# Performance work log

Measured on AMD Instinct MI355X. Metric: run time of the kernel, lower is better.

## Reference

```python
import jax, jax.numpy as jnp
import numpy as np
from jax import lax

BATCH, FS, DIM = 32, 7, 512
E, TOPK, KD = 4, 2, 4            # experts, top-k, scan directions
N_STATE, DT_RANK = 16, 32
CAP_FACTOR, EPS, AUX_W = 1.25, 1e-6, 0.01


def _layernorm(x, g, b, eps=1e-5):
    mu = x.mean(-1, keepdims=True)
    var = ((x - mu) ** 2).mean(-1, keepdims=True)
    return (x - mu) * lax.rsqrt(var + eps) * g + b


def setup_inputs() -> dict:
    key = jax.random.key(0)
    ks = jax.random.split(key, 10)
    s = 0.02
    d = DIM
    return {
        "x": jax.random.normal(ks[0], (BATCH, FS, FS, d), jnp.float32),
        "w_gate": jax.random.normal(ks[1], (d, E)) * s,
        "b_gate": jnp.zeros((E,), jnp.float32),
        "in_proj_w": jax.random.normal(ks[2], (E, d, 2 * d)) * s,
        "in_proj_b": jnp.zeros((E, 2 * d), jnp.float32),
        "conv_w": jax.random.normal(ks[3], (E, d, 3, 3)) * s,
        "conv_b": jnp.zeros((E, d), jnp.float32),
        "x_proj_w": jax.random.normal(ks[4], (E, KD, DT_RANK + 2 * N_STATE, d)) * s,
        "dt_proj_w": jax.random.normal(ks[5], (E, KD, d, DT_RANK)) * s,
        "dt_proj_b": jax.random.normal(ks[6], (E, KD, d)) * 0.1,
        "A_log": jnp.log(jax.random.uniform(ks[7], (E, KD, d, N_STATE), minval=1.0, maxval=16.0)),
        "Ds": jnp.ones((E, KD, d), jnp.float32),
        "out_norm_g": jnp.ones((E, d), jnp.float32),
        "out_norm_b": jnp.zeros((E, d), jnp.float32),
        "norm_g": jnp.ones((E, d), jnp.float32),
        "norm_b": jnp.zeros((E, d), jnp.float32),
    }


def _ss2d_expert(x, in_w, in_b, cw, cb, xpw, dtw, dtb, A_log, Ds, og, ob, ng, nb):
    # x: [B,H,W,d]; one SS2D expert (VMamba-style, use_out_proj=False, out_norm=True)
    B, H, W, d = x.shape
    L = H * W
    xz = x @ in_w + in_b                      # [B,H,W,2d]
    xin, z = jnp.split(xz, 2, axis=-1)
    xc = jnp.transpose(xin, (0, 3, 1, 2))     # [B,d,H,W]
    xc = lax.conv_general_dilated(xc, cw[:, None, :, :], (1, 1), 'SAME',
                                  feature_group_count=d,
                                  dimension_numbers=('NCHW', 'OIHW', 'NCHW'))
    xc = jax.nn.silu(xc + cb[None, :, None, None])
    xh = xc.reshape(B, d, L)                              # row-major (h)
    xv = jnp.transpose(xc, (0, 1, 3, 2)).reshape(B, d, L)  # col-major (v)
    xs = jnp.stack([xh, xh[..., ::-1], xv, xv[..., ::-1]], axis=1)  # [B,K,d,L]

    x_dbl = jnp.einsum('bkdl,kcd->bkcl', xs, xpw)
    dt, Bm, Cm = jnp.split(x_dbl, [DT_RANK, DT_RANK + N_STATE], axis=2)
    dt = jnp.einsum('bkrl,kdr->bkdl', dt, dtw) + dtb[None, :, :, None]
    dt = jax.nn.softplus(dt)                  # [B,K,d,L]
    A = -jnp.exp(A_log)                       # [K,d,N]

    def step(h, inp):
        dt_t, B_t, C_t, x_t = inp             # [B,K,d],[B,K,N],[B,K,N],[B,K,d]
        h = h * jnp.exp(dt_t[..., None] * A) + (dt_t * x_t)[..., None] * B_t[:, :, None, :]
        y = jnp.einsum('bkdn,bkn->bkd', h, C_t)
        return h, y

    h0 = jnp.zeros((B, KD, d, N_STATE), x.dtype)
    seq = (jnp.moveaxis(dt, 3, 0), jnp.moveaxis(Bm, 3, 0),
           jnp.moveaxis(Cm, 3, 0), jnp.moveaxis(xs, 3, 0))
    _, ys = lax.scan(step, h0, seq)           # [L,B,K,d]
    ys = jnp.moveaxis(ys, 0, 3) + Ds[None, :, :, None] * xs  # [B,K,d,L]

    y = ys[:, 0] + ys[:, 1, :, ::-1]
    yv = ys[:, 2] + ys[:, 3, :, ::-1]
    y = y + jnp.transpose(yv.reshape(B, d, W, H), (0, 1, 3, 2)).reshape(B, d, L)
    y = jnp.transpose(y.reshape(B, d, H, W), (0, 2, 3, 1))   # [B,H,W,d]
    y = _layernorm(y, og, ob) * jax.nn.silu(z)
    pooled = y.mean(axis=(1, 2))              # adaptive avg pool -> [B,d]
    return _layernorm(pooled, ng, nb)


def reference(x, w_gate, b_gate, in_proj_w, in_proj_b, conv_w, conv_b, x_proj_w,
              dt_proj_w, dt_proj_b, A_log, Ds, out_norm_g, out_norm_b, norm_g, norm_b):
    B = x.shape[0]
    # gate on globally pooled features
    x_flat = x.mean(axis=(1, 2))                              # [B,dim]
    raw = jax.nn.softmax(x_flat @ w_gate + b_gate, axis=-1)   # [B,E]
    capacity = int(CAP_FACTOR * B)
    _, idx = lax.top_k(raw, TOPK)
    mask = jax.nn.one_hot(idx, E, dtype=raw.dtype).sum(axis=1)  # [B,E]
    masked = raw * mask
    denom = masked.sum(0, keepdims=True) + EPS
    gate_scores = masked / denom * capacity
    importance = raw.mean(0)
    load = mask.mean(0)
    aux_loss = AUX_W * jnp.mean((load - importance) ** 2)

    topv, topi = lax.top_k(gate_scores, TOPK)                 # [B,k]
    # dense dispatch: run every expert on the full batch (E small), then gather
    all_out = jax.vmap(_ss2d_expert, in_axes=(None,) + (0,) * 13)(
        x, in_proj_w, in_proj_b, conv_w, conv_b, x_proj_w, dt_proj_w, dt_proj_b,
        A_log, Ds, out_norm_g, out_norm_b, norm_g, norm_b)    # [E,B,dim]
    sel = all_out[topi, jnp.arange(B)[:, None]]               # [B,k,dim]
    mixed = (topv[..., None] * sel).sum(axis=1)               # [B,dim]
    return mixed, aux_loss
```

## Files before the change

### kernel.cpp

```cpp
#include <hip/hip_runtime.h>
#include <hip/hip_bf16.h>

#define B_   32
#define D_   512
#define L_   49
#define E_   4
#define KD_  4
#define NS_  16
#define RK_  32
#define JOBS_ 64

typedef short s16x8 __attribute__((ext_vector_type(8)));
typedef float f32x4v __attribute__((ext_vector_type(4)));
union U4 { uint4 u; s16x8 s; unsigned short us[8]; };

__device__ __forceinline__ float bf2f(unsigned short u){
  union{unsigned int i; float f;} v; v.i = ((unsigned int)u)<<16; return v.f;
}
__device__ __forceinline__ float2 bfp(unsigned int u){
  union{unsigned int i; float f;} a, b; a.i = u<<16; b.i = u & 0xffff0000u;
  return make_float2(a.f, b.f);
}
__device__ __forceinline__ unsigned short f2bfu(float f){
  union{float f; unsigned int i;} u; u.f = f;
  unsigned int r = u.i + 0x7fffu + ((u.i >> 16) & 1u);
  return (unsigned short)(r >> 16);
}
__device__ __forceinline__ float silu_f(float x){ return x / (1.f + expf(-x)); }

__device__ __forceinline__ float fast_exp2(float x){
  return __builtin_amdgcn_exp2f(x);
}
__device__ __forceinline__ float quad_add4(float y){
  float t1 = __uint_as_float(__builtin_amdgcn_mov_dpp(__float_as_uint(y), 0xB1, 0xF, 0xF, true));
  y += t1;
  float t2 = __uint_as_float(__builtin_amdgcn_mov_dpp(__float_as_uint(y), 0x4E, 0xF, 0xF, true));
  y += t2;
  return y;
}
__device__ __forceinline__ unsigned cvtpk_bf16(float lo, float hi){
  unsigned r; asm("v_cvt_pk_bf16_f32 %0, %1, %2" : "=v"(r) : "v"(lo), "v"(hi)); return r;
}

__device__ __forceinline__ int detect_bf(const void* x){
  unsigned short u = ((const unsigned short*)x)[threadIdx.x & 63];
  int e = (u >> 7) & 0xff;
  unsigned long long m = __ballot(e >= 96 && e < 160);
  return __popcll(m) >= 56;
}

__device__ __forceinline__ float ldf(const void* p, size_t i, int bf){
  return bf ? bf2f(((const unsigned short*)p)[i]) : ((const float*)p)[i];
}
struct f8s{ float v[8]; };
__device__ __forceinline__ f8s ldf8(const void* p, size_t i, int bf){
  f8s r;
  if (bf){
    uint4 u = *(const uint4*)((const unsigned short*)p + i);
    float2 x = bfp(u.x), y = bfp(u.y), z = bfp(u.z), w = bfp(u.w);
    r.v[0]=x.x; r.v[1]=x.y; r.v[2]=y.x; r.v[3]=y.y;
    r.v[4]=z.x; r.v[5]=z.y; r.v[6]=w.x; r.v[7]=w.y;
  } else {
    const float4* q = (const float4*)((const float*)p + i);
    float4 a = q[0], b = q[1];
    r.v[0]=a.x; r.v[1]=a.y; r.v[2]=a.z; r.v[3]=a.w;
    r.v[4]=b.x; r.v[5]=b.y; r.v[6]=b.z; r.v[7]=b.w;
  }
  return r;
}
struct f4s{ float v[4]; };
__device__ __forceinline__ f4s ldf4(const void* p, size_t i, int bf){
  f4s r;
  if (bf){
    uint2 u = *(const uint2*)((const unsigned short*)p + i);
    float2 a = bfp(u.x), b = bfp(u.y);
    r.v[0]=a.x; r.v[1]=a.y; r.v[2]=b.x; r.v[3]=b.y;
  } else {
    float4 a = *(const float4*)((const float*)p + i);
    r.v[0]=a.x; r.v[1]=a.y; r.v[2]=a.z; r.v[3]=a.w;
  }
  return r;
}
__device__ __forceinline__ U4 ldbf8(const void* p, size_t i, int bf){
  U4 r;
  if (bf){
    r.u = *(const uint4*)((const unsigned short*)p + i);
  } else {
    const float* q = (const float*)p + i;
    float4 a = *(const float4*)q, b = *(const float4*)(q+4);
    r.u.x = (unsigned)f2bfu(a.x) | ((unsigned)f2bfu(a.y) << 16);
    r.u.y = (unsigned)f2bfu(a.z) | ((unsigned)f2bfu(a.w) << 16);
    r.u.z = (unsigned)f2bfu(b.x) | ((unsigned)f2bfu(b.y) << 16);
    r.u.w = (unsigned)f2bfu(b.z) | ((unsigned)f2bfu(b.w) << 16);
  }
  return r;
}
__device__ __forceinline__ void split8(const float av[8], U4& hi, U4& lo){
  #pragma unroll
  for (int j = 0; j < 8; j++){
    union{float f; unsigned int i;} u; u.f = av[j];
    unsigned short h = (unsigned short)(u.i >> 16);
    hi.us[j] = h;
    lo.us[j] = f2bfu(av[j] - bf2f(h));
  }
}

__device__ __forceinline__ int dirmap(int k, int l){
  if (k == 0) return l;
  if (k == 1) return 48 - l;
  if (k == 2) return (l % 7) * 7 + l / 7;
  int l2 = 48 - l; return (l2 % 7) * 7 + l2 / 7;
}

__global__ __launch_bounds__(256) void k_prep(const void* __restrict__ x,
                                              const void* __restrict__ w,
                                              const void* __restrict__ wg,
                                              const void* __restrict__ bg,
                                              unsigned short* __restrict__ wt,
                                              unsigned short* __restrict__ xbf,
                                              float* __restrict__ logits){
  __shared__ unsigned short tile[64][72];
  __shared__ float red[4][4];
  __shared__ float pool[4][512];
  int bf = detect_bf(x);
  int blk = blockIdx.x;
  int t = threadIdx.x;
  if (blk < 512){
    int e = blk >> 7, cb = (blk >> 3) & 15, db = blk & 7;
    #pragma unroll
    for (int r = 0; r < 4; r++){
      int d  = r*16 + (t>>4);
      int c0 = (t&15)*4;
      size_t g = ((size_t)e*512 + db*64 + d)*1024 + cb*64 + c0;
      if (bf){
        uint2 u = *(const uint2*)((const unsigned short*)w + g);
        tile[c0+0][d] = (unsigned short)(u.x & 0xffffu);
        tile[c0+1][d] = (unsigned short)(u.x >> 16);
        tile[c0+2][d] = (unsigned short)(u.y & 0xffffu);
        tile[c0+3][d] = (unsigned short)(u.y >> 16);
      } else {
        float4 v = *(const float4*)((const float*)w + g);
        tile[c0+0][d] = f2bfu(v.x);
        tile[c0+1][d] = f2bfu(v.y);
        tile[c0+2][d] = f2bfu(v.z);
        tile[c0+3][d] = f2bfu(v.w);
      }
    }
    __syncthreads();
    #pragma unroll
    for (int r = 0; r < 2; r++){
      int o = r*256 + t;
      int c = o >> 3, d0 = (o & 7)*8;
      uint4 v = *(const uint4*)&tile[c][d0];
      *(uint4*)(wt + ((size_t)e*1024 + cb*64 + c)*512 + db*64 + d0) = v;
    }
  } else {
    int b = blk - 512;
    int wave = t >> 6, lane = t & 63;
    int d0 = lane * 8;
    float s8[8] = {};
    for (int l = wave; l < L_; l += 4){
      size_t ix = ((size_t)(b*L_ + l))*D_ + d0;
      U4 xb;
      if (bf){
        xb.u = *(const uint4*)((const unsigned short*)x + ix);
        float2 a = bfp(xb.u.x), bq = bfp(xb.u.y), c = bfp(xb.u.z), dq = bfp(xb.u.w);
        s8[0] += a.x;  s8[1] += a.y;  s8[2] += bq.x; s8[3] += bq.y;
        s8[4] += c.x;  s8[5] += c.y;  s8[6] += dq.x; s8[7] += dq.y;
      } else {
        const float* q = (const float*)x + ix;
        float4 f0 = *(const float4*)q, f1 = *(const float4*)(q+4);
        float av[8] = {f0.x,f0.y,f0.z,f0.w, f1.x,f1.y,f1.z,f1.w};
        #pragma unroll
        for (int j = 0; j < 8; j++){ xb.us[j] = f2bfu(av[j]); s8[j] += av[j]; }
      }
      *(uint4*)(xbf + ix) = xb.u;
    }
    #pragma unroll
    for (int j = 0; j < 8; j++) pool[wave][d0+j] = s8[j];
    __syncthreads();
    float p[4] = {0.f, 0.f, 0.f, 0.f};
    #pragma unroll
    for (int rep = 0; rep < 2; rep++){
      int d = t + rep*256;
      float s = pool[0][d] + pool[1][d] + pool[2][d] + pool[3][d];
      float xfd = s * (1.f/49.f);
      #pragma unroll
      for (int e = 0; e < 4; e++) p[e] = fmaf(xfd, ldf(wg, (size_t)d*E_ + e, bf), p[e]);
    }
    #pragma unroll
    for (int off = 32; off > 0; off >>= 1){
      #pragma unroll
      for (int e = 0; e < 4; e++) p[e] += __shfl_down(p[e], off, 64);
    }
    if (lane == 0){
      #pragma unroll
      for (int e = 0; e < 4; e++) red[wave][e] = p[e];
    }
    __syncthreads();
    if (t < 4)
      logits[b*4 + t] = red[0][t]+red[1][t]+red[2][t]+red[3][t] + ldf(bg, t, bf);
  }
}

__global__ __launch_bounds__(128) void k_gate2(const void* __restrict__ x,
                                               const float* __restrict__ logits,
                                               int* __restrict__ topi, float* __restrict__ topv,
                                               void* __restrict__ out){
  __shared__ float raw[B_*E_];
  __shared__ int   sel[B_];
  __shared__ float den[E_], auxp[E_];
  int bf = detect_bf(x);
  int t = threadIdx.x;
  if (t < B_){
    float l0=logits[t*4+0], l1=logits[t*4+1], l2=logits[t*4+2], l3=logits[t*4+3];
    float m = fmaxf(fmaxf(l0,l1), fmaxf(l2,l3));
    float e0=expf(l0-m), e1=expf(l1-m), e2=expf(l2-m), e3=expf(l3-m);
    float s = e0+e1+e2+e3;
    float r[4] = {e0/s, e1/s, e2/s, e3/s};
    int i1 = 0; float v1 = r[0];
    for (int e = 1; e < 4; e++) if (r[e] > v1){ v1 = r[e]; i1 = e; }
    int i2 = -1; float v2 = -1.f;
    for (int e = 0; e < 4; e++){ if (e == i1) continue; if (r[e] > v2){ v2 = r[e]; i2 = e; } }
    if (i1 < 0 || i1 > 3) i1 = 0;
    if (i2 < 0 || i2 > 3) i2 = (i1 + 1) & 3;
    sel[t] = (1<<i1) | (1<<i2);
    for (int e = 0; e < 4; e++) raw[t*4+e] = r[e];
  }
  __syncthreads();
  if (t < E_){
    float dn = 0.f, imp = 0.f, ld = 0.f;
    for (int b = 0; b < B_; b++){
      float r = raw[b*4+t];
      int bit = (sel[b] >> t) & 1;
      if (bit) dn += r;
      imp += r; ld += (float)bit;
    }
    den[t] = dn + 1e-6f;
    imp *= (1.f/B_); ld *= (1.f/B_);
    float df = ld - imp; auxp[t] = df*df;
  }
  __syncthreads();
  if (t == 0){
    float a = 0.01f * 0.25f * (auxp[0]+auxp[1]+auxp[2]+auxp[3]);
    if (bf) ((unsigned short*)out)[16384] = f2bfu(a);
    else    ((float*)out)[16384] = a;
  }
  if (t < B_){
    float gs[4];
    for (int e = 0; e < 4; e++){
      int bit = (sel[t] >> e) & 1;
      gs[e] = bit ? raw[t*4+e] * 40.f / den[e] : 0.f;
    }
    int i1 = 0; float v1 = gs[0];
    for (int e = 1; e < 4; e++) if (gs[e] > v1){ v1 = gs[e]; i1 = e; }
    int i2 = -1; float v2 = -1e30f;
    for (int e = 0; e < 4; e++){ if (e == i1) continue; if (gs[e] > v2){ v2 = gs[e]; i2 = e; } }
    if (i1 < 0 || i1 > 3) i1 = 0;
    if (i2 < 0 || i2 > 3) i2 = (i1 + 1) & 3;
    topi[t*2+0] = i1; topv[t*2+0] = v1;
    topi[t*2+1] = i2; topv[t*2+1] = v2;
  }
}

__global__ __launch_bounds__(256, 4) void k_inproj_mfma(const void* __restrict__ x,
                                                     const unsigned short* __restrict__ xbf,
                                                     const unsigned short* __restrict__ wt,
                                                     const void* __restrict__ bias,
                                                     const void* __restrict__ cw,
                                                     const void* __restrict__ cb,
                                                     const int* __restrict__ topi,
                                                     unsigned short* __restrict__ zbuf,
                                                     float* __restrict__ xc,
                                                     unsigned short* __restrict__ xchi,
                                                     unsigned short* __restrict__ xclo){
  __shared__ unsigned short smem[2*4096];
  float* xzt = (float*)smem;
  int bf = detect_bf(x);
  int job = blockIdx.x, nt = blockIdx.y;
  int b = job >> 1;
  int e = topi[job];
  int t = threadIdx.x;
  int wave = t >> 6, lane = t & 63;
  int l16 = lane & 15, quad = lane >> 4;
  int arow = wave*16 + l16; if (arow > 48) arow = 48;
  size_t abase = ((size_t)(b*L_ + arow))*D_;
  int ct = nt*64;
  const unsigned short* wsrc = wt + (size_t)(e*1024 + ct)*512;
  f32x4v acc[4] = {};
  #pragma unroll
  for (int cc = 0; cc < 2; cc++){
    int c = t + cc*256;
    int col = c >> 3, ko8 = c & 7;
    uint4 v = *(const uint4*)(wsrc + (size_t)col*512 + ko8*8);
    *(uint4*)(smem + col*64 + ((ko8 ^ (col & 7))*8)) = v;
  }
  U4 aA, aB;
  aA.u = *(const uint4*)(xbf + abase + quad*8);
  aB.u = *(const uint4*)(xbf + abase + 32 + quad*8);
  __syncthreads();
  for (int s = 0; s < 8; s++){
    unsigned short* cur = smem + (s & 1)*4096;
    U4 nA, nB;
    if (s < 7){
      unsigned short* nxt = smem + ((s+1) & 1)*4096;
      int k0n = (s+1)*64;
      #pragma unroll
      for (int cc = 0; cc < 2; cc++){
        int c = t + cc*256;
        int col = c >> 3, ko8 = c & 7;
        uint4 v = *(const uint4*)(wsrc + (size_t)col*512 + k0n + ko8*8);
        *(uint4*)(nxt + col*64 + ((ko8 ^ (col & 7))*8)) = v;
      }
      nA.u = *(const uint4*)(xbf + abase + k0n + quad*8);
      nB.u = *(const uint4*)(xbf + abase + k0n + 32 + quad*8);
    }
    {
      int ko8 = quad;
      #pragma unroll
      for (int ss = 0; ss < 4; ss++){
        int col = ss*16 + l16;
        U4 bb; bb.u = *(const uint4*)(cur + col*64 + ((ko8 ^ (col & 7))*8));
        acc[ss] = __builtin_amdgcn_mfma_f32_16x16x32_bf16(aA.s, bb.s, acc[ss], 0, 0, 0);
      }
      ko8 = 4 + quad;
      #pragma unroll
      for (int ss = 0; ss < 4; ss++){
        int col = ss*16 + l16;
        U4 bb; bb.u = *(const uint4*)(cur + col*64 + ((ko8 ^ (col & 7))*8));
        acc[ss] = __builtin_amdgcn_mfma_f32_16x16x32_bf16(aB.s, bb.s, acc[ss], 0, 0, 0);
      }
    }
    aA = nA; aB = nB;
    __syncthreads();
  }
  int rb = wave*16 + quad*4;
  if (nt >= 8){
    #pragma unroll
    for (int s = 0; s < 4; s++){
      int c = ct + s*16 + l16;
      float bv = ldf(bias, (size_t)e*1024 + c, bf);
      #pragma unroll
      for (int r = 0; r < 4; r++){
        int row = rb + r;
        if (row < L_)
          zbuf[(size_t)job*25088 + row*D_ + (c - 512)] = f2bfu(acc[s][r] + bv);
      }
    }
    return;
  }
  #pragma unroll
  for (int s = 0; s < 4; s++){
    int cl = s*16 + l16;
    float bv = ldf(bias, (size_t)e*1024 + ct + cl, bf);
    #pragma unroll
    for (int r = 0; r < 4; r++){
      int row = rb + r;
      if (row < L_) xzt[row*68 + cl] = acc[s][r] + bv;
    }
  }
  __syncthreads();
  int c = t & 63, pg = t >> 6;
  int dch = ct + c;
  float wv[9];
  #pragma unroll
  for (int j = 0; j < 9; j++) wv[j] = ldf(cw, ((size_t)(e*D_ + dch))*9 + j, bf);
  float cbv = ldf(cb, (size_t)e*D_ + dch, bf);
  for (int p = pg; p < L_; p += 4){
    int h = p / 7, w = p % 7;
    float a2 = cbv;
    #pragma unroll
    for (int dy = 0; dy < 3; dy++){
      int hh = h + dy - 1; if (hh < 0 || hh >= 7) continue;
      #pragma unroll
      for (int dx = 0; dx < 3; dx++){
        int ww = w + dx - 1; if (ww < 0 || ww >= 7) continue;
        a2 = fmaf(xzt[(hh*7+ww)*68 + c], wv[dy*3+dx], a2);
      }
    }
    float sv = a2 * (1.f/(1.f+expf(-a2)));
    size_t oix = (size_t)job*25088 + (size_t)p*D_ + dch;
    xc[oix] = sv;
    unsigned int ui = __float_as_uint(sv);
    unsigned short hh2 = (unsigned short)(ui >> 16);
    xchi[oix] = hh2;
    xclo[oix] = f2bfu(sv - bf2f(hh2));
  }
}

__global__ __launch_bounds__(256, 4) void k_xproj(const void* __restrict__ x,
                                               const void* __restrict__ xpw,
                                               const int* __restrict__ topi,
                                               const unsigned short* __restrict__ xchi,
                                               const unsigned short* __restrict__ xclo,
                                               float* __restrict__ xdbl){
  int bf = detect_bf(x);
  int kq = blockIdx.x, job = blockIdx.y;
  int k = kq & 3, q = kq >> 2;
  int t = threadIdx.x;
  int wave = t >> 6, lane = t & 63;
  int l16 = lane & 15, quad = lane >> 4;
  int e = topi[job];
  int arow = q*16 + l16; if (arow > 48) arow = 48;
  int m = dirmap(k, arow);
  const unsigned short* ahp = xchi + (size_t)job*25088 + (size_t)m*D_;
  const unsigned short* alp = xclo + (size_t)job*25088 + (size_t)m*D_;
  size_t bbase = (((size_t)(e*KD_+k))*64 + wave*16 + l16)*D_;
  f32x4v acc = {};
  #pragma unroll
  for (int k0 = 0; k0 < 512; k0 += 32){
    int kk = k0 + quad*8;
    U4 Ahi, Alo;
    Ahi.u = *(const uint4*)(ahp + kk);
    Alo.u = *(const uint4*)(alp + kk);
    U4 bb = ldbf8(xpw, bbase + kk, bf);
    acc = __builtin_amdgcn_mfma_f32_16x16x32_bf16(Ahi.s, bb.s, acc, 0, 0, 0);
    acc = __builtin_amdgcn_mfma_f32_16x16x32_bf16(Alo.s, bb.s, acc, 0, 0, 0);
  }
  float* outb = xdbl + ((size_t)(job*KD_+k))*3136;
  int rb = q*16 + quad*4;
  int c = wave*16 + l16;
  #pragma unroll
  for (int r = 0; r < 4; r++){
    int row = rb + r;
    if (row < L_) outb[row*64 + c] = acc[r];
  }
}

__global__ __launch_bounds__(256, 2) void k_scan(const void* __restrict__ x,
                                              const void* __restrict__ dtw,
                                              const void* __restrict__ dtb_,
                                              const void* __restrict__ alog,
                                              const void* __restrict__ ds_,
                                              const int* __restrict__ topi,
                                              const float* __restrict__ xc,
                                              const float* __restrict__ xdbl,
                                              unsigned short* __restrict__ ybuf){
  int bf = detect_bf(x);
  int kz = blockIdx.x, job = blockIdx.y;
  int k = kz & 3, dz2 = kz >> 2;
  int t = threadIdx.x;
  int e = topi[job];
  int ek = e*KD_ + k;
  __shared__ float bc[49*32];
  __shared__ float dtl[49*260];
  const float* xdb = xdbl + ((size_t)(job*KD_+k))*3136;
  {
    const float4* src4 = (const float4*)xdb;
    for (int i = t; i < 392; i += 256){
      int row = i >> 3, c = i & 7;
      ((float4*)bc)[row*8 + c] = src4[row*16 + 8 + c];
    }
  }
  int w = t >> 6, lane = t & 63;
  {
    int l16 = lane & 15, quad4 = lane >> 4;
    U4 Bv[4];
    #pragma unroll
    for (int nt = 0; nt < 4; nt++){
      int d = dz2*256 + w*64 + nt*16 + l16;
      Bv[nt] = ldbf8(dtw, ((size_t)ek*D_ + d)*RK_ + quad4*8, bf);
    }
    f32x4v acc[4][4] = {};
    #pragma unroll
    for (int rt = 0; rt < 4; rt++){
      int arow = rt*16 + l16; if (arow > 48) arow = 48;
      const float* ap = xdb + arow*64 + quad4*8;
      float4 f0 = *(const float4*)ap, f1 = *(const float4*)(ap+4);
      float av[8] = {f0.x,f0.y,f0.z,f0.w, f1.x,f1.y,f1.z,f1.w};
      U4 Ahi, Alo;
      split8(av, Ahi, Alo);
      #pragma unroll
      for (int nt = 0; nt < 4; nt++){
        acc[rt][nt] = __builtin_amdgcn_mfma_f32_16x16x32_bf16(Ahi.s, Bv[nt].s, acc[rt][nt], 0, 0, 0);
        acc[rt][nt] = __builtin_amdgcn_mfma_f32_16x16x32_bf16(Alo.s, Bv[nt].s, acc[rt][nt], 0, 0, 0);
      }
    }
    #pragma unroll
    for (int nt = 0; nt < 4; nt++){
      int d = dz2*256 + w*64 + nt*16 + l16;
      float bias = ldf(dtb_, (size_t)ek*D_ + d, bf);
      int dloc = w*64 + nt*16 + l16;
      #pragma unroll
      for (int rt = 0; rt < 4; rt++){
        #pragma unroll
        for (int r = 0; r < 4; r++){
          int l = rt*16 + quad4*4 + r;
          if (l < L_){
            float v = acc[rt][nt][r] + bias;
            dtl[l*260 + dloc] = fmaxf(v, 0.f) + __logf(1.f + __expf(-fabsf(v)));
          }
        }
      }
    }
  }
  int q4 = (lane >> 2) * 4;
  int ng = lane & 3;
  int dgl = dz2*256 + w*64 + q4;
  float A2[4][4], Dsv[4];
  #pragma unroll
  for (int jj = 0; jj < 4; jj++){
    int dj = dgl + jj;
    f4s ar = ldf4(alog, ((size_t)ek*D_ + dj)*NS_ + ng*4, bf);
    #pragma unroll
    for (int n = 0; n < 4; n++) A2[jj][n] = -expf(ar.v[n]) * 1.44269504f;
    Dsv[jj] = ldf(ds_, (size_t)ek*D_ + dj, bf);
  }
  __syncthreads();
  float h[4][4];
  #pragma unroll
  for (int jj = 0; jj < 4; jj++)
    #pragma unroll
    for (int n = 0; n < 4; n++) h[jj][n] = 0.f;
  const float* xcb = xc + (size_t)job*25088;
  unsigned short* yb = ybuf + ((size_t)(job*KD_ + k))*25088;
  int dtbase = w*64 + q4;
  for (int c0 = 0; c0 < 49; c0 += 7){
    float4 xv[7];
    #pragma unroll
    for (int j = 0; j < 7; j++){
      int m = dirmap(k, c0 + j);
      xv[j] = *(const float4*)(xcb + (size_t)m*D_ + dgl);
    }
    #pragma unroll
    for (int j = 0; j < 7; j++){
      int l = c0 + j;
      float4 dt4 = *(const float4*)&dtl[l*260 + dtbase];
      float4 B4 = *(const float4*)&bc[l*32 + ng*4];
      float4 C4 = *(const float4*)&bc[l*32 + 16 + ng*4];
      float Ba[4] = {B4.x, B4.y, B4.z, B4.w};
      float Ca[4] = {C4.x, C4.y, C4.z, C4.w};
      float dta[4] = {dt4.x, dt4.y, dt4.z, dt4.w};
      float xa[4]  = {xv[j].x, xv[j].y, xv[j].z, xv[j].w};
      float ys[4];
      #pragma unroll
      for (int jj = 0; jj < 4; jj++){
        float dt = dta[jj], x_t = xa[jj];
        float dtx = dt * x_t;
        float y = 0.f;
        #pragma unroll
        for (int n = 0; n < 4; n++){
          float en = fast_exp2(dt * A2[jj][n]);
          h[jj][n] = fmaf(h[jj][n], en, dtx * Ba[n]);
          y = fmaf(h[jj][n], Ca[n], y);
        }
        y = quad_add4(y);
        ys[jj] = fmaf(Dsv[jj], x_t, y);
      }
      if (ng == 0){
        uint2 o;
        o.x = cvtpk_bf16(ys[0], ys[1]);
        o.y = cvtpk_bf16(ys[2], ys[3]);
        *(uint2*)(yb + (size_t)l*D_ + dgl) = o;
      }
    }
  }
}

__global__ __launch_bounds__(512) void k_final_a(const void* __restrict__ x,
                                                 const void* __restrict__ og,
                                                 const void* __restrict__ ob,
                                                 const int* __restrict__ topi,
                                                 const unsigned short* __restrict__ ybuf,
                                                 const unsigned short* __restrict__ zbuf,
                                                 float* __restrict__ partial){
  __shared__ float pool[8][512];
  int bf = detect_bf(x);
  int job = blockIdx.x, q = blockIdx.y, t = threadIdx.x;
  int wave = t >> 6, lane = t & 63;
  int e = topi[job];
  int d0 = lane*8;
  const unsigned short* yb = ybuf + (size_t)job*KD_*25088;
  const unsigned short* zb = zbuf + (size_t)job*25088;
  float g[8], o[8];
  {
    f8s gg = ldf8(og, (size_t)e*D_ + d0, bf);
    f8s oo = ldf8(ob, (size_t)e*D_ + d0, bf);
    #pragma unroll
    for (int j = 0; j < 8; j++){ g[j] = gg.v[j]; o[j] = oo.v[j]; }
  }
  float acc[8] = {};
  for (int i = wave; i <= 12; i += 8){
    int p = q + 4*i;
    if (p >= L_) break;
    float v[8] = {};
    #pragma unroll
    for (int k = 0; k < KD_; k++){
      int l = dirmap(k, p);
      U4 r; r.u = *(const uint4*)(yb + (size_t)k*25088 + (size_t)l*D_ + d0);
      #pragma unroll
      for (int j = 0; j < 8; j++) v[j] += bf2f(r.us[j]);
    }
    float s = 0.f, ss = 0.f;
    #pragma unroll
    for (int j = 0; j < 8; j++){ s += v[j]; ss += v[j]*v[j]; }
    #pragma unroll
    for (int off = 32; off > 0; off >>= 1){
      s  += __shfl_xor(s,  off, 64);
      ss += __shfl_xor(ss, off, 64);
    }
    float mu = s*(1.f/512.f);
    float var = ss*(1.f/512.f) - mu*mu;
    float rs = rsqrtf(var + 1e-5f);
    U4 zz; zz.u = *(const uint4*)(zb + (size_t)p*D_ + d0);
    #pragma unroll
    for (int j = 0; j < 8; j++){
      float zv = bf2f(zz.us[j]);
      acc[j] += ((v[j]-mu)*rs*g[j] + o[j]) * silu_f(zv);
    }
  }
  #pragma unroll
  for (int j = 0; j < 8; j++) pool[wave][d0+j] = acc[j];
  __syncthreads();
  float pd = pool[0][t]+pool[1][t]+pool[2][t]+pool[3][t]
           + pool[4][t]+pool[5][t]+pool[6][t]+pool[7][t];
  partial[((size_t)(job*4 + q))*512 + t] = pd;
}

__global__ __launch_bounds__(512) void k_finmix(const void* __restrict__ x,
                                                const void* __restrict__ ngg,
                                                const void* __restrict__ nbb,
                                                const int* __restrict__ topi,
                                                const float* __restrict__ topv,
                                                const float* __restrict__ partial,
                                                void* __restrict__ out){
  __shared__ float red[32];
  int bf = detect_bf(x);
  int b = blockIdx.x, t = threadIdx.x;
  int wave = t >> 6, lane = t & 63;
  int j0 = 2*b, j1 = 2*b + 1;
  int e0 = topi[j0], e1 = topi[j1];
  float g0 = topv[j0], g1 = topv[j1];
  const float* p0 = partial + (size_t)j0*4*512;
  const float* p1 = partial + (size_t)j1*4*512;
  float pd0 = (p0[t] + p0[512+t] + p0[1024+t] + p0[1536+t]) * (1.f/49.f);
  float pd1 = (p1[t] + p1[512+t] + p1[1024+t] + p1[1536+t]) * (1.f/49.f);
  float s0 = pd0, ss0 = pd0*pd0, s1 = pd1, ss1 = pd1*pd1;
  #pragma unroll
  for (int off = 32; off > 0; off >>= 1){
    s0  += __shfl_down(s0,  off, 64);
    ss0 += __shfl_down(ss0, off, 64);
    s1  += __shfl_down(s1,  off, 64);
    ss1 += __shfl_down(ss1, off, 64);
  }
  if (lane == 0){
    red[wave] = s0; red[8+wave] = ss0; red[16+wave] = s1; red[24+wave] = ss1;
  }
  __syncthreads();
  s0 = red[0]+red[1]+red[2]+red[3]+red[4]+red[5]+red[6]+red[7];
  ss0 = red[8]+red[9]+red[10]+red[11]+red[12]+red[13]+red[14]+red[15];
  s1 = red[16]+red[17]+red[18]+red[19]+red[20]+red[21]+red[22]+red[23];
  ss1 = red[24]+red[25]+red[26]+red[27]+red[28]+red[29]+red[30]+red[31];
  float mu0 = s0*(1.f/512.f), var0 = ss0*(1.f/512.f) - mu0*mu0;
  float rs0 = rsqrtf(var0 + 1e-5f);
  float mu1 = s1*(1.f/512.f), var1 = ss1*(1.f/512.f) - mu1*mu1;
  float rs1 = rsqrtf(var1 + 1e-5f);
  float v0 = ((pd0-mu0)*rs0*ldf(ngg, (size_t)e0*D_+t, bf) + ldf(nbb, (size_t)e0*D_+t, bf)) * g0;
  float v1 = ((pd1-mu1)*rs1*ldf(ngg, (size_t)e1*D_+t, bf) + ldf(nbb, (size_t)e1*D_+t, bf)) * g1;
  float v = v0 + v1;
  if (bf) ((unsigned short*)out)[b*D_ + t] = f2bfu(v);
  else    ((float*)out)[b*D_ + t] = v;
}

extern "C" void kernel_launch(void* const* d_in, const int* in_sizes, int n_in,
                              void* d_out, int out_size, void* d_ws, size_t ws_size,
                              hipStream_t stream){
  const void* x    = d_in[0];
  const void* wg   = d_in[1];
  const void* bg   = d_in[2];
  const void* ipw  = d_in[3];
  const void* ipb  = d_in[4];
  const void* cw   = d_in[5];
  const void* cb   = d_in[6];
  const void* xpw  = d_in[7];
  const void* dtw  = d_in[8];
  const void* dtb  = d_in[9];
  const void* alog = d_in[10];
  const void* dss  = d_in[11];
  const void* ogg  = d_in[12];
  const void* obb  = d_in[13];
  const void* ngg  = d_in[14];
  const void* nbb  = d_in[15];
  float* wsf = (float*)d_ws;
  int*   topi  = (int*)d_ws + 16;
  float* topv  = wsf + 96;
  float* logits= wsf + 256;
  float* xc    = wsf + 16640;
  float* xdbl  = wsf + 1622272;
  unsigned short* zbuf = (unsigned short*)(wsf + 2425088);
  unsigned short* ybuf   = (unsigned short*)(wsf + 3260672);
  unsigned short* wtrans = ybuf;
  unsigned short* xchi   = ybuf + 2097152;
  unsigned short* xclo   = ybuf + 3702784;
  unsigned short* xbf    = ybuf + 5308416;
  float* partial = wsf + 6471936;

  k_prep  <<<544, 256, 0, stream>>>(x, ipw, wg, bg, wtrans, xbf, logits);
  k_gate2 <<<1, 128, 0, stream>>>(x, logits, topi, topv, d_out);
  k_inproj_mfma<<<dim3(64,16), 256, 0, stream>>>(x, xbf, wtrans, ipb, cw, cb, topi, zbuf, xc, xchi, xclo);
  k_xproj <<<dim3(16,64), 256, 0, stream>>>(x, xpw, topi, xchi, xclo, xdbl);
  k_scan  <<<dim3(8,64), 256, 0, stream>>>(x, dtw, dtb, alog, dss, topi, xc, xdbl, ybuf);
  k_final_a<<<dim3(64,4), 512, 0, stream>>>(x, ogg, obb, topi, ybuf, zbuf, partial);
  k_finmix<<<32, 512, 0, stream>>>(x, ngg, nbb, topi, topv, partial, d_out);
}
```

Before: 201.0 us.

## Double-buffer xproj weight tiles through swizzled LDS with register prefetch

The x_proj kernel now stages 64-column by 64-k chunks of the bf16 weight into a double-buffered, XOR-swizzled shared-memory tile, cooperatively loaded by all threads. It also prefetches the next chunk's A fragments into registers while the current chunk's MFMAs run. The goal is to overlap global loads with compute and replace the per-lane strided weight reads with coalesced ones. In exchange it adds LDS use and a barrier per iteration, and this kernel is small relative to the whole pipeline.

Result: faster. 191.2 us, median of 3 (-4.9%).

```diff
diff --git a/kernel.cpp b/kernel.cpp
--- a/kernel.cpp
+++ b/kernel.cpp
@@ -394,6 +394,7 @@
                                                const unsigned short* __restrict__ xchi,
                                                const unsigned short* __restrict__ xclo,
                                                float* __restrict__ xdbl){
+  __shared__ unsigned short smem[2*4096];
   int bf = detect_bf(x);
   int kq = blockIdx.x, job = blockIdx.y;
   int k = kq & 3, q = kq >> 2;
@@ -405,17 +406,52 @@
   int m = dirmap(k, arow);
   const unsigned short* ahp = xchi + (size_t)job*25088 + (size_t)m*D_;
   const unsigned short* alp = xclo + (size_t)job*25088 + (size_t)m*D_;
-  size_t bbase = (((size_t)(e*KD_+k))*64 + wave*16 + l16)*D_;
+  size_t bsrc = ((size_t)(e*KD_+k))*64*512;
+  int col16 = wave*16 + l16;
   f32x4v acc = {};
   #pragma unroll
-  for (int k0 = 0; k0 < 512; k0 += 32){
-    int kk = k0 + quad*8;
-    U4 Ahi, Alo;
-    Ahi.u = *(const uint4*)(ahp + kk);
-    Alo.u = *(const uint4*)(alp + kk);
-    U4 bb = ldbf8(xpw, bbase + kk, bf);
-    acc = __builtin_amdgcn_mfma_f32_16x16x32_bf16(Ahi.s, bb.s, acc, 0, 0, 0);
-    acc = __builtin_amdgcn_mfma_f32_16x16x32_bf16(Alo.s, bb.s, acc, 0, 0, 0);
+  for (int cc = 0; cc < 2; cc++){
+    int c = t + cc*256;
+    int col = c >> 3, ko8 = c & 7;
+    U4 v = ldbf8(xpw, bsrc + (size_t)col*512 + ko8*8, bf);
+    *(uint4*)(smem + col*64 + ((ko8 ^ (col & 7))*8)) = v.u;
+  }
+  U4 hA, hB, lA, lB;
+  hA.u = *(const uint4*)(ahp + quad*8);
+  lA.u = *(const uint4*)(alp + quad*8);
+  hB.u = *(const uint4*)(ahp + 32 + quad*8);
+  lB.u = *(const uint4*)(alp + 32 + quad*8);
+  __syncthreads();
+  for (int s = 0; s < 8; s++){
+    unsigned short* cur = smem + (s & 1)*4096;
+    U4 nhA, nhB, nlA, nlB;
+    if (s < 7){
+      unsigned short* nxt = smem + ((s+1) & 1)*4096;
+      int k0n = (s+1)*64;
+      #pragma unroll
+      for (int cc = 0; cc < 2; cc++){
+        int c = t + cc*256;
+        int col = c >> 3, ko8 = c & 7;
+        U4 v = ldbf8(xpw, bsrc + (size_t)col*512 + k0n + ko8*8, bf);
+        *(uint4*)(nxt + col*64 + ((ko8 ^ (col & 7))*8)) = v.u;
+      }
+      nhA.u = *(const uint4*)(ahp + k0n + quad*8);
+      nlA.u = *(const uint4*)(alp + k0n + quad*8);
+      nhB.u = *(const uint4*)(ahp + k0n + 32 + quad*8);
+      nlB.u = *(const uint4*)(alp + k0n + 32 + quad*8);
+    }
+    {
+      int ko8 = quad;
+      U4 bb;  bb.u  = *(const uint4*)(cur + col16*64 + ((ko8 ^ (col16 & 7))*8));
+      acc = __builtin_amdgcn_mfma_f32_16x16x32_bf16(hA.s, bb.s, acc, 0, 0, 0);
+      acc = __builtin_amdgcn_mfma_f32_16x16x32_bf16(lA.s, bb.s, acc, 0, 0, 0);
+      ko8 = 4 + quad;
+      U4 bb2; bb2.u = *(const uint4*)(cur + col16*64 + ((ko8 ^ (col16 & 7))*8));
+      acc = __builtin_amdgcn_mfma_f32_16x16x32_bf16(hB.s, bb2.s, acc, 0, 0, 0);
+      acc = __builtin_amdgcn_mfma_f32_16x16x32_bf16(lB.s, bb2.s, acc, 0, 0, 0);
+    }
+    hA = nhA; hB = nhB; lA = nlA; lB = nlB;
+    __syncthreads();
   }
   float* outb = xdbl + ((size_t)(job*KD_+k))*3136;
   int rb = q*16 + quad*4;
```
